# Performance work log

Hardware: AMD Instinct MI355X
Metric: run time of the kernel (lower is better)

Reference implementation:

```python
import jax, jax.numpy as jnp
import numpy as np

B, H, S, D = 2, 16, 2048, 64

def setup_inputs() -> dict:
    key = jax.random.key(0)
    kq, kk, kv = jax.random.split(key, 3)
    q = jax.random.normal(kq, (B, H, S, D), dtype=jnp.float32)
    k = jax.random.normal(kk, (B, H, S, D), dtype=jnp.float32)
    v = jax.random.normal(kv, (B, H, S, D), dtype=jnp.float32)
    return {"q": q, "k": k, "v": v}

def reference(q, k, v):
    scale = q.shape[-1] ** -0.5
    # sim: [b, h, i, j]
    sim = jnp.einsum('bhid,bhjd->bhij', q, k) * scale
    attn = jax.nn.softmax(sim, axis=-1)
    out = jnp.einsum('bhij,bhjd->bhid', attn, v)
    return out
```

## Files before the change

### kernel.cpp

```cpp
#include <hip/hip_runtime.h>

typedef _Float16 f16;
typedef f16 f16x4 __attribute__((ext_vector_type(4)));
typedef f16 f16x8 __attribute__((ext_vector_type(8)));
typedef float f32x4 __attribute__((ext_vector_type(4)));

static constexpr int S_LEN  = 2048;
static constexpr int D_DIM  = 64;
static constexpr int NTILE  = 64;
static constexpr int MBLOCK = 128;
static constexpr int KST    = 72;
static constexpr int VST    = 72;
static constexpr float SCALE_LOG2E = 0.1803368801111204f;
static constexpr float SHIFT = 4.0f;

#define MFMA32(a,b,c) __builtin_amdgcn_mfma_f32_16x16x32_f16((a),(b),(c),0,0,0)
#define MFMA16(a,b,c) __builtin_amdgcn_mfma_f32_16x16x16f16((a),(b),(c),0,0,0)

__global__ __launch_bounds__(256, 2)
void attn_fwd(const float* __restrict__ qg, const float* __restrict__ kg,
              const float* __restrict__ vg, float* __restrict__ og) {
  const int xcd  = blockIdx.x & 7;
  const int slot = blockIdx.x >> 3;
  const int bh   = xcd * 4 + (slot >> 4);
  const int qt   = slot & 15;
  const size_t hbase = (size_t)bh * S_LEN * D_DIM;
  const float* qh = qg + hbase;
  const float* kh = kg + hbase;
  const float* vh = vg + hbase;
  float*       oh = og + hbase;

  const int tid  = threadIdx.x;
  const int wave = tid >> 6;
  const int lane = tid & 63;
  const int L    = lane & 15;
  const int quad = lane >> 4;
  const int lhalf = L >> 3;

  __shared__ f16 Ks[2][NTILE * KST];
  __shared__ f16 Vt[2][D_DIM * VST];

  f16x8 qf[2][2];
  const int qrow0 = qt * MBLOCK + wave * 32;
#pragma unroll
  for (int qs = 0; qs < 2; ++qs)
#pragma unroll
    for (int kc = 0; kc < 2; ++kc) {
      const float* src = qh + (size_t)(qrow0 + qs * 16 + L) * D_DIM + kc * 32 + quad * 8;
      float4 x0 = *(const float4*)src;
      float4 x1 = *(const float4*)(src + 4);
      f16x8 t;
      t[0] = (f16)x0.x; t[1] = (f16)x0.y; t[2] = (f16)x0.z; t[3] = (f16)x0.w;
      t[4] = (f16)x1.x; t[5] = (f16)x1.y; t[6] = (f16)x1.z; t[7] = (f16)x1.w;
      qf[qs][kc] = t;
    }

  f32x4 oacc[2][4];
#pragma unroll
  for (int qs = 0; qs < 2; ++qs)
#pragma unroll
    for (int dt = 0; dt < 4; ++dt) oacc[qs][dt] = (f32x4){0.f, 0.f, 0.f, 0.f};
  float lsum[2] = {0.f, 0.f};

  const int sj  = tid >> 2, sc  = tid & 3;
  const int jd  = tid >> 4, dcc = tid & 15;
  const int vpos = ((jd & 3) * 4 + (jd >> 2)) * 4;
  const int xorv = (dcc >> 1) << 3;
  const float* kstage = kh + (size_t)sj * D_DIM + sc * 4;
  const float* vstage = vh + (size_t)(jd * 4) * D_DIM + dcc * 4;

  float4 kreg[4], vreg[4];

#pragma unroll
  for (int i = 0; i < 4; ++i) {
    kreg[i] = *(const float4*)(kstage + i * 16);
    vreg[i] = *(const float4*)(vstage + (size_t)i * D_DIM);
  }
#pragma unroll
  for (int i = 0; i < 4; ++i) {
    f16x4 t;
    t[0] = (f16)kreg[i].x; t[1] = (f16)kreg[i].y;
    t[2] = (f16)kreg[i].z; t[3] = (f16)kreg[i].w;
    *(f16x4*)&Ks[0][sj * KST + i * 16 + sc * 4] = t;
  }
  {
    const float* vr = reinterpret_cast<const float*>(vreg);
#pragma unroll
    for (int c = 0; c < 4; ++c) {
      f16x4 t;
      t[0] = (f16)vr[0 * 4 + c]; t[1] = (f16)vr[1 * 4 + c];
      t[2] = (f16)vr[2 * 4 + c]; t[3] = (f16)vr[3 * 4 + c];
      *(f16x4*)&Vt[0][(dcc * 4 + c) * VST + (vpos ^ xorv)] = t;
    }
  }
#pragma unroll
  for (int i = 0; i < 4; ++i) {
    kreg[i] = *(const float4*)(kstage + (size_t)1 * NTILE * D_DIM + i * 16);
    vreg[i] = *(const float4*)(vstage + (size_t)1 * NTILE * D_DIM + (size_t)i * D_DIM);
  }
  __syncthreads();

  constexpr int NT = S_LEN / NTILE;
  for (int kt = 0; kt < NT; ++kt) {
    const int cur = kt & 1;
    const int nxt = cur ^ 1;

    f32x4 sfr[2][4];
#pragma unroll
    for (int qs = 0; qs < 2; ++qs)
#pragma unroll
      for (int jt = 0; jt < 4; ++jt) sfr[qs][jt] = (f32x4){0.f, 0.f, 0.f, 0.f};
#pragma unroll
    for (int jt = 0; jt < 4; ++jt)
#pragma unroll
      for (int kc = 0; kc < 2; ++kc) {
        f16x8 af = *(const f16x8*)&Ks[cur][(jt * 16 + L) * KST + kc * 32 + quad * 8];
        sfr[0][jt] = MFMA32(af, qf[0][kc], sfr[0][jt]);
        sfr[1][jt] = MFMA32(af, qf[1][kc], sfr[1][jt]);
      }

    if (kt + 1 < NT) {
#pragma unroll
      for (int i = 0; i < 4; ++i) {
        f16x4 t;
        t[0] = (f16)kreg[i].x; t[1] = (f16)kreg[i].y;
        t[2] = (f16)kreg[i].z; t[3] = (f16)kreg[i].w;
        *(f16x4*)&Ks[nxt][sj * KST + i * 16 + sc * 4] = t;
      }
      const float* vr = reinterpret_cast<const float*>(vreg);
#pragma unroll
      for (int c = 0; c < 4; ++c) {
        f16x4 t;
        t[0] = (f16)vr[0 * 4 + c]; t[1] = (f16)vr[1 * 4 + c];
        t[2] = (f16)vr[2 * 4 + c]; t[3] = (f16)vr[3 * 4 + c];
        *(f16x4*)&Vt[nxt][(dcc * 4 + c) * VST + (vpos ^ xorv)] = t;
      }
    }
    if (kt + 2 < NT) {
      const float* kp = kstage + (size_t)(kt + 2) * NTILE * D_DIM;
      const float* vp = vstage + (size_t)(kt + 2) * NTILE * D_DIM;
#pragma unroll
      for (int i = 0; i < 4; ++i) {
        kreg[i] = *(const float4*)(kp + i * 16);
        vreg[i] = *(const float4*)(vp + (size_t)i * D_DIM);
      }
    }

    f16x4 pf[2][4];
#pragma unroll
    for (int qs = 0; qs < 2; ++qs)
#pragma unroll
      for (int jt = 0; jt < 4; ++jt) {
#pragma unroll
        for (int r = 0; r < 4; ++r) {
          const float p = __builtin_amdgcn_exp2f(
              __builtin_fmaf(sfr[qs][jt][r], SCALE_LOG2E, -SHIFT));
          lsum[qs] += p;
          pf[qs][jt][r] = (f16)p;
        }
      }

#pragma unroll
    for (int jtp = 0; jtp < 2; ++jtp)
#pragma unroll
      for (int dt = 0; dt < 4; ++dt) {
        const int xorr = ((2 * dt + lhalf) & 7) << 3;
        f16x8 vf = *(const f16x8*)&Vt[cur][(dt * 16 + L) * VST +
                                          ((quad * 16 + jtp * 8) ^ xorr)];
        f16x4 vlo = {vf[0], vf[1], vf[2], vf[3]};
        f16x4 vhi = {vf[4], vf[5], vf[6], vf[7]};
        oacc[0][dt] = MFMA16(pf[0][jtp * 2],     vlo, oacc[0][dt]);
        oacc[0][dt] = MFMA16(pf[0][jtp * 2 + 1], vhi, oacc[0][dt]);
        oacc[1][dt] = MFMA16(pf[1][jtp * 2],     vlo, oacc[1][dt]);
        oacc[1][dt] = MFMA16(pf[1][jtp * 2 + 1], vhi, oacc[1][dt]);
      }

    __syncthreads();
  }

#pragma unroll
  for (int qs = 0; qs < 2; ++qs) {
    float l = lsum[qs];
    l += __shfl_xor(l, 16);
    l += __shfl_xor(l, 32);
#pragma unroll
    for (int r = 0; r < 4; ++r) {
      const float inv = 1.0f / __shfl(l, quad * 4 + r);
      float* dst = oh + (size_t)(qrow0 + qs * 16 + quad * 4 + r) * D_DIM + L;
#pragma unroll
      for (int dt = 0; dt < 4; ++dt)
        dst[dt * 16] = oacc[qs][dt][r] * inv;
    }
  }
}

extern "C" void kernel_launch(void* const* d_in, const int* in_sizes, int n_in,
                              void* d_out, int out_size, void* d_ws, size_t ws_size,
                              hipStream_t stream) {
  const float* q = (const float*)d_in[0];
  const float* k = (const float*)d_in[1];
  const float* v = (const float*)d_in[2];
  float* o = (float*)d_out;
  dim3 grid(32 * (S_LEN / MBLOCK));
  dim3 block(256);
  attn_fwd<<<grid, block, 0, stream>>>(q, k, v, o);
}
```

Before: 131.3 us.

## Prepack K/V to swizzled fp16 and stream tiles via global_load_lds

Adds a prepack kernel that converts K and V to fp16 in a pre-swizzled, pre-transposed tile layout in the workspace. The attention kernel then copies each tile straight into LDS with global_load_lds, which removes the per-tile register staging, conversion and transposed LDS writes, and halves the bytes each of the 16 query blocks per head reads for K/V. In exchange it adds a second kernel launch and a full extra pass over K and V, and falls back to the old kernel if the workspace is too small.

```diff
diff --git a/kernel.cpp b/kernel.cpp
--- a/kernel.cpp
+++ b/kernel.cpp
@@ -9,17 +9,205 @@
 static constexpr int D_DIM  = 64;
 static constexpr int NTILE  = 64;
 static constexpr int MBLOCK = 128;
-static constexpr int KST    = 72;
-static constexpr int VST    = 72;
 static constexpr float SCALE_LOG2E = 0.1803368801111204f;
 static constexpr float SHIFT = 4.0f;
 
 #define MFMA32(a,b,c) __builtin_amdgcn_mfma_f32_16x16x32_f16((a),(b),(c),0,0,0)
 #define MFMA16(a,b,c) __builtin_amdgcn_mfma_f32_16x16x16f16((a),(b),(c),0,0,0)
 
+#define GLOAD_LDS16(gptr, lptr)                                          \
+  __builtin_amdgcn_global_load_lds(                                      \
+      (const __attribute__((address_space(1))) void*)(gptr),             \
+      (__attribute__((address_space(3))) void*)(lptr), 16, 0, 0)
+
+__global__ __launch_bounds__(256)
+void prepack(const float* __restrict__ kg, const float* __restrict__ vg,
+             f16* __restrict__ kp, f16* __restrict__ vp) {
+  int b = blockIdx.x;
+  const bool isV = (b >= 1024);
+  if (isV) b -= 1024;
+  const int head = b >> 5;
+  const int tile = b & 31;
+  const int t = threadIdx.x;
+  const size_t base = ((size_t)head * S_LEN + (size_t)tile * NTILE) * D_DIM;
+
+  if (!isV) {
+    const float* src = kg + base;
+    f16* dst = kp + base;
+#pragma unroll
+    for (int e = 0; e < 2; ++e) {
+      const int ch = t * 2 + e;
+      const int j = ch >> 3, c = ch & 7;
+      const int cp = c ^ (j & 7);
+      const float* s = src + j * D_DIM + c * 8;
+      float4 a0 = *(const float4*)s;
+      float4 a1 = *(const float4*)(s + 4);
+      f16x8 o;
+      o[0] = (f16)a0.x; o[1] = (f16)a0.y; o[2] = (f16)a0.z; o[3] = (f16)a0.w;
+      o[4] = (f16)a1.x; o[5] = (f16)a1.y; o[6] = (f16)a1.z; o[7] = (f16)a1.w;
+      *(f16x8*)(dst + j * 64 + cp * 8) = o;
+    }
+  } else {
+    const float* src = vg + base;
+    f16* dst = vp + base;
+#pragma unroll
+    for (int e = 0; e < 2; ++e) {
+      const int ch = t * 2 + e;
+      const int j = ch >> 3, c = ch & 7;
+      const int jtp = j >> 5, rem = j & 31;
+      const int hi16 = rem >> 4, quad = (rem & 15) >> 2, i = rem & 3;
+      const int cl = quad * 2 + jtp;
+      const int s_in = hi16 * 4 + i;
+      const float* s = src + j * D_DIM + c * 8;
+      float4 a0 = *(const float4*)s;
+      float4 a1 = *(const float4*)(s + 4);
+      const float v8[8] = {a0.x, a0.y, a0.z, a0.w, a1.x, a1.y, a1.z, a1.w};
+#pragma unroll
+      for (int dd = 0; dd < 8; ++dd) {
+        const int d = c * 8 + dd;
+        const int cp = cl ^ (d & 7);
+        dst[d * 64 + cp * 8 + s_in] = (f16)v8[dd];
+      }
+    }
+  }
+}
+
 __global__ __launch_bounds__(256, 2)
-void attn_fwd(const float* __restrict__ qg, const float* __restrict__ kg,
-              const float* __restrict__ vg, float* __restrict__ og) {
+void attn_pp(const float* __restrict__ qg, const f16* __restrict__ kp,
+             const f16* __restrict__ vp, float* __restrict__ og) {
+  const int xcd  = blockIdx.x & 7;
+  const int slot = blockIdx.x >> 3;
+  const int bh   = xcd * 4 + (slot >> 4);
+  const int qt   = slot & 15;
+  const size_t hbase = (size_t)bh * S_LEN * D_DIM;
+  const float* qh = qg + hbase;
+  const f16*   kh = kp + hbase;
+  const f16*   vh = vp + hbase;
+  float*       oh = og + hbase;
+
+  const int tid  = threadIdx.x;
+  const int wave = tid >> 6;
+  const int lane = tid & 63;
+  const int L    = lane & 15;
+  const int quad = lane >> 4;
+  const int l7   = L & 7;
+
+  __shared__ f16 Ks[2][NTILE * D_DIM];
+  __shared__ f16 Vt[2][NTILE * D_DIM];
+
+  f16x8 qf[2][2];
+  const int qrow0 = qt * MBLOCK + wave * 32;
+#pragma unroll
+  for (int qs = 0; qs < 2; ++qs)
+#pragma unroll
+    for (int kc = 0; kc < 2; ++kc) {
+      const float* src = qh + (size_t)(qrow0 + qs * 16 + L) * D_DIM + kc * 32 + quad * 8;
+      float4 x0 = *(const float4*)src;
+      float4 x1 = *(const float4*)(src + 4);
+      f16x8 t;
+      t[0] = (f16)x0.x; t[1] = (f16)x0.y; t[2] = (f16)x0.z; t[3] = (f16)x0.w;
+      t[4] = (f16)x1.x; t[5] = (f16)x1.y; t[6] = (f16)x1.z; t[7] = (f16)x1.w;
+      qf[qs][kc] = t;
+    }
+
+  f32x4 oacc[2][4];
+#pragma unroll
+  for (int qs = 0; qs < 2; ++qs)
+#pragma unroll
+    for (int dt = 0; dt < 4; ++dt) oacc[qs][dt] = (f32x4){0.f, 0.f, 0.f, 0.f};
+  float lsum[2] = {0.f, 0.f};
+
+#define STAGE(buf, kt_)                                                    \
+  do {                                                                     \
+    const char* kb = (const char*)(kh + (size_t)(kt_) * 4096);             \
+    const char* vb = (const char*)(vh + (size_t)(kt_) * 4096);             \
+    _Pragma("unroll")                                                      \
+    for (int c = 0; c < 2; ++c) {                                          \
+      const int off = wave * 2048 + c * 1024;                              \
+      GLOAD_LDS16(kb + off + lane * 16, (char*)&Ks[buf][0] + off);         \
+      GLOAD_LDS16(vb + off + lane * 16, (char*)&Vt[buf][0] + off);         \
+    }                                                                      \
+  } while (0)
+
+  STAGE(0, 0);
+  __syncthreads();
+
+  constexpr int NT = S_LEN / NTILE;
+  for (int kt = 0; kt < NT; ++kt) {
+    const int cur = kt & 1;
+    const int nxt = cur ^ 1;
+
+    if (kt + 1 < NT) STAGE(nxt, kt + 1);
+
+    f32x4 sfr[2][4];
+#pragma unroll
+    for (int qs = 0; qs < 2; ++qs)
+#pragma unroll
+      for (int jt = 0; jt < 4; ++jt) sfr[qs][jt] = (f32x4){0.f, 0.f, 0.f, 0.f};
+#pragma unroll
+    for (int jt = 0; jt < 4; ++jt)
+#pragma unroll
+      for (int kc = 0; kc < 2; ++kc) {
+        f16x8 af = *(const f16x8*)&Ks[cur][(jt * 16 + L) * 64 +
+                                          (((kc * 4 + quad) ^ l7) * 8)];
+        sfr[0][jt] = MFMA32(af, qf[0][kc], sfr[0][jt]);
+        sfr[1][jt] = MFMA32(af, qf[1][kc], sfr[1][jt]);
+      }
+
+    f16x4 pf[2][4];
+#pragma unroll
+    for (int qs = 0; qs < 2; ++qs)
+#pragma unroll
+      for (int jt = 0; jt < 4; ++jt) {
+#pragma unroll
+        for (int r = 0; r < 4; ++r) {
+          const float p = __builtin_amdgcn_exp2f(
+              __builtin_fmaf(sfr[qs][jt][r], SCALE_LOG2E, -SHIFT));
+          lsum[qs] += p;
+          pf[qs][jt][r] = (f16)p;
+        }
+      }
+
+#pragma unroll
+    for (int jtp = 0; jtp < 2; ++jtp)
+#pragma unroll
+      for (int dt = 0; dt < 4; ++dt) {
+        f16x8 vf = *(const f16x8*)&Vt[cur][(dt * 16 + L) * 64 +
+                                          (((quad * 2 + jtp) ^ l7) * 8)];
+        f16x4 vlo = {vf[0], vf[1], vf[2], vf[3]};
+        f16x4 vhi = {vf[4], vf[5], vf[6], vf[7]};
+        oacc[0][dt] = MFMA16(pf[0][jtp * 2],     vlo, oacc[0][dt]);
+        oacc[0][dt] = MFMA16(pf[0][jtp * 2 + 1], vhi, oacc[0][dt]);
+        oacc[1][dt] = MFMA16(pf[1][jtp * 2],     vlo, oacc[1][dt]);
+        oacc[1][dt] = MFMA16(pf[1][jtp * 2 + 1], vhi, oacc[1][dt]);
+      }
+
+    __syncthreads();
+  }
+#undef STAGE
+
+#pragma unroll
+  for (int qs = 0; qs < 2; ++qs) {
+    float l = lsum[qs];
+    l += __shfl_xor(l, 16);
+    l += __shfl_xor(l, 32);
+#pragma unroll
+    for (int r = 0; r < 4; ++r) {
+      const float inv = 1.0f / __shfl(l, quad * 4 + r);
+      float* dst = oh + (size_t)(qrow0 + qs * 16 + quad * 4 + r) * D_DIM + L;
+#pragma unroll
+      for (int dt = 0; dt < 4; ++dt)
+        dst[dt * 16] = oacc[qs][dt][r] * inv;
+    }
+  }
+}
+
+static constexpr int KST = 72;
+static constexpr int VST = 72;
+
+__global__ __launch_bounds__(256, 2)
+void attn_fwd_fb(const float* __restrict__ qg, const float* __restrict__ kg,
+                 const float* __restrict__ vg, float* __restrict__ og) {
   const int xcd  = blockIdx.x & 7;
   const int slot = blockIdx.x >> 3;
   const int bh   = xcd * 4 + (slot >> 4);
@@ -70,7 +258,6 @@
   const float* vstage = vh + (size_t)(jd * 4) * D_DIM + dcc * 4;
 
   float4 kreg[4], vreg[4];
-
 #pragma unroll
   for (int i = 0; i < 4; ++i) {
     kreg[i] = *(const float4*)(kstage + i * 16);
@@ -137,12 +324,12 @@
       }
     }
     if (kt + 2 < NT) {
-      const float* kp = kstage + (size_t)(kt + 2) * NTILE * D_DIM;
-      const float* vp = vstage + (size_t)(kt + 2) * NTILE * D_DIM;
+      const float* kpp = kstage + (size_t)(kt + 2) * NTILE * D_DIM;
+      const float* vpp = vstage + (size_t)(kt + 2) * NTILE * D_DIM;
 #pragma unroll
       for (int i = 0; i < 4; ++i) {
-        kreg[i] = *(const float4*)(kp + i * 16);
-        vreg[i] = *(const float4*)(vp + (size_t)i * D_DIM);
+        kreg[i] = *(const float4*)(kpp + i * 16);
+        vreg[i] = *(const float4*)(vpp + (size_t)i * D_DIM);
       }
     }
 
@@ -201,7 +388,16 @@
   const float* k = (const float*)d_in[1];
   const float* v = (const float*)d_in[2];
   float* o = (float*)d_out;
-  dim3 grid(32 * (S_LEN / MBLOCK));
-  dim3 block(256);
-  attn_fwd<<<grid, block, 0, stream>>>(q, k, v, o);
+
+  const size_t kv_elems = (size_t)32 * S_LEN * D_DIM;
+  const size_t need = 2 * kv_elems * sizeof(f16);
+
+  if (ws_size >= need && d_ws != nullptr) {
+    f16* kp = (f16*)d_ws;
+    f16* vp = kp + kv_elems;
+    prepack<<<dim3(2048), dim3(256), 0, stream>>>(k, v, kp, vp);
+    attn_pp<<<dim3(512), dim3(256), 0, stream>>>(q, kp, vp, o);
+  } else {
+    attn_fwd_fb<<<dim3(512), dim3(256), 0, stream>>>(q, k, v, o);
+  }
 }
```

Result: slower. 140.2 us (+6.8%).
